# Kernel optimization log

Hardware: AMD Instinct MI355X
Metric: run time of the kernel (lower is better)

## Reference

```python
import jax, jax.numpy as jnp
import numpy as np

N, E = 20000, 320000          # nodes, edges
R, B = 9, 9                   # num_relations, num_bases
IN, HID, OUT = 128, 256, 64   # feature dims
EPS = 1e-5                    # LayerNorm eps


def layer_norm(h, gamma, beta):
    mu = jnp.mean(h, axis=-1, keepdims=True)
    var = jnp.var(h, axis=-1, keepdims=True)
    return (h - mu) * jax.lax.rsqrt(var + EPS) * gamma + beta


def rgcn_conv(x, src, dst, etype, bases, comp, root, bias, aggr):
    # basis decomposition: W_r = sum_b comp[r,b] * bases[b]
    W = jnp.einsum('rb,bio->rio', comp, bases)          # [R, in, out]
    xW = jnp.einsum('ni,rio->rno', x, W)                # [R, N, out]
    msg = xW[etype, src]                                # [E, out] gather per edge
    if aggr == 'max':
        agg = jax.ops.segment_max(msg, dst, num_segments=N)
        agg = jnp.where(jnp.isfinite(agg), agg, 0.0)    # empty segments -> 0
    else:
        agg = jax.ops.segment_sum(msg, dst, num_segments=N)
    return agg + x @ root + bias


def setup_inputs() -> dict:
    key = jax.random.key(0)
    ks = jax.random.split(key, 12)
    rn = lambda k, s, sc=0.05: jax.random.normal(k, s, jnp.float32) * sc
    return {
        'x': jax.random.normal(ks[0], (N, IN), jnp.float32),
        'edge_index': jax.random.randint(ks[1], (2, E), 0, N),
        'edge_type': jax.random.randint(ks[2], (E,), 0, R),
        # conv1 params
        'bases1': rn(ks[3], (B, IN, HID)),
        'comp1': rn(ks[4], (R, B), 0.3),
        'root1': rn(ks[5], (IN, HID)),
        'bias1': jnp.zeros((HID,), jnp.float32),
        'g1': jnp.ones((HID,), jnp.float32),
        'b1': jnp.zeros((HID,), jnp.float32),
        # conv2 params
        'bases2': rn(ks[6], (B, HID, OUT)),
        'comp2': rn(ks[7], (R, B), 0.3),
        'root2': rn(ks[8], (HID, OUT)),
        'bias2': jnp.zeros((OUT,), jnp.float32),
        'g2': jnp.ones((OUT,), jnp.float32),
        'b2': jnp.zeros((OUT,), jnp.float32),
    }


def reference(x, edge_index, edge_type, bases1, comp1, root1, bias1, g1, b1,
              bases2, comp2, root2, bias2, g2, b2):
    src, dst = edge_index[0], edge_index[1]
    h = rgcn_conv(x, src, dst, edge_type, bases1, comp1, root1, bias1, 'max')
    h = jax.nn.relu(layer_norm(h, g1, b1))
    # eval mode: edge dropout and feature dropout are identity
    h = rgcn_conv(h, src, dst, edge_type, bases2, comp2, root2, bias2, 'add')
    h = layer_norm(h, g2, b2)
    return jax.nn.log_softmax(h, axis=1)
```

## Files before the change

kernel.cpp:

```cpp
#include <hip/hip_runtime.h>
#include <math.h>

#define NN 20000
#define NE 320000
#define NREL 9
#define NBASES 9
#define D_IN 128
#define D_HID 256
#define D_OUT 64
#define LN_EPS 1e-5f

#define N1 (NREL * D_HID + D_HID)
#define N2 (NREL * D_OUT + D_OUT)
#define NBLK ((NN + 255) / 256)

typedef __attribute__((ext_vector_type(8))) short bf16x8;
typedef __attribute__((ext_vector_type(4))) float f32x4;

__device__ inline ushort f2b(float f) {
    unsigned u = __float_as_uint(f);
    return (ushort)((u + 0x7FFFu + ((u >> 16) & 1u)) >> 16);
}
__device__ inline float b2f(ushort h) { return __uint_as_float(((unsigned)h) << 16); }
__device__ inline unsigned pack2bf(float f0, float f1) {
    return (unsigned)f2b(f0) | ((unsigned)f2b(f1) << 16);
}

__global__ __launch_bounds__(256) void prep_all(
    const float* __restrict__ bases1, const float* __restrict__ comp1, const float* __restrict__ root1,
    const float* __restrict__ bases2, const float* __restrict__ comp2, const float* __restrict__ root2,
    const float* __restrict__ x, const int* __restrict__ dst,
    ushort* __restrict__ w1t, ushort* __restrict__ w2t, ushort* __restrict__ xbf,
    int* __restrict__ deg)
{
    const int SZW1 = D_IN * D_HID;
    const int SZW2 = D_HID * D_OUT;
    const int SZX  = NN * D_IN;
    int tid = blockIdx.x * 256 + threadIdx.x;
    if (tid < SZW1) {
        int o = tid & (D_HID - 1), k = tid >> 8;
        float acc[NREL];
        #pragma unroll
        for (int r = 0; r < NREL; r++) acc[r] = 0.f;
        #pragma unroll
        for (int b = 0; b < NBASES; b++) {
            float bs = bases1[(b * D_IN + k) * D_HID + o];
            #pragma unroll
            for (int r = 0; r < NREL; r++) acc[r] += comp1[r * NBASES + b] * bs;
        }
        #pragma unroll
        for (int r = 0; r < NREL; r++)
            w1t[(r * D_HID + o) * D_IN + k] = f2b(acc[r]);
        w1t[(NREL * D_HID + o) * D_IN + k] = f2b(root1[k * D_HID + o]);
    } else if (tid < SZW1 + SZW2) {
        int j = tid - SZW1;
        int o = j & (D_OUT - 1), k = j >> 6;
        float acc[NREL];
        #pragma unroll
        for (int r = 0; r < NREL; r++) acc[r] = 0.f;
        #pragma unroll
        for (int b = 0; b < NBASES; b++) {
            float bs = bases2[(b * D_HID + k) * D_OUT + o];
            #pragma unroll
            for (int r = 0; r < NREL; r++) acc[r] += comp2[r * NBASES + b] * bs;
        }
        #pragma unroll
        for (int r = 0; r < NREL; r++)
            w2t[(r * D_OUT + o) * D_HID + k] = f2b(acc[r]);
        w2t[(NREL * D_OUT + o) * D_HID + k] = f2b(root2[k * D_OUT + o]);
    } else if (tid < SZW1 + SZW2 + SZX) {
        int j = tid - SZW1 - SZW2;
        xbf[j] = f2b(x[j]);
    } else if (tid < SZW1 + SZW2 + SZX + NE) {
        int e = tid - SZW1 - SZW2 - SZX;
        atomicAdd(&deg[dst[e]], 1);
    }
}

__global__ __launch_bounds__(256) void scan_blk(
    const int* __restrict__ deg, int* __restrict__ local, int* __restrict__ bsum)
{
    __shared__ int wsum[4];
    int tid = threadIdx.x, lane = tid & 63, w = tid >> 6;
    int i = blockIdx.x * 256 + tid;
    int v = (i < NN) ? deg[i] : 0;
    int x = v;
    #pragma unroll
    for (int d = 1; d < 64; d <<= 1) {
        int y = __shfl_up(x, d, 64);
        if (lane >= d) x += y;
    }
    if (lane == 63) wsum[w] = x;
    __syncthreads();
    int woff = 0;
    for (int j = 0; j < w; j++) woff += wsum[j];
    if (i < NN) local[i] = woff + x - v;
    if (tid == 255) bsum[blockIdx.x] = woff + x;
}

__global__ __launch_bounds__(256) void scan_fin(
    const int* __restrict__ local, const int* __restrict__ bsum,
    int* __restrict__ offs, int* __restrict__ cursor)
{
    __shared__ int boff_s[NBLK];
    int tid = threadIdx.x;
    if (tid < 64) {
        int carry = 0;
        for (int base = 0; base < NBLK; base += 64) {
            int i = base + tid;
            int v = (i < NBLK) ? bsum[i] : 0;
            int x = v;
            #pragma unroll
            for (int d = 1; d < 64; d <<= 1) {
                int y = __shfl_up(x, d, 64);
                if (tid >= d) x += y;
            }
            if (i < NBLK) boff_s[i] = carry + x - v;
            carry += __shfl(x, 63, 64);
        }
    }
    __syncthreads();
    int i = blockIdx.x * 256 + tid;
    if (i < NN) {
        int o = local[i] + boff_s[i >> 8];
        offs[i] = o;
        cursor[i] = o;
    }
    if (i == NN) offs[NN] = NE;
}

__global__ __launch_bounds__(256) void scatter_ep(
    const int* __restrict__ src, const int* __restrict__ dst, const int* __restrict__ etype,
    int* __restrict__ cursor, int* __restrict__ ep1)
{
    int e = blockIdx.x * 256 + threadIdx.x;
    if (e >= NE) return;
    int d = dst[e];
    int s = src[e], r = etype[e];
    int pos = atomicAdd(&cursor[d], 1);
    ep1[pos] = s * N1 + r * D_HID;
}

__global__ __launch_bounds__(256) void gemm_bf16(
    const ushort* __restrict__ A, const ushort* __restrict__ Bt, ushort* __restrict__ C,
    int M, int N, int K)
{
    __shared__ ushort As[2][512 * 8];
    __shared__ ushort Bs[2][512 * 8];

    int tid = threadIdx.x;
    int lane = tid & 63, w = tid >> 6;
    int wm = w >> 1, wn = w & 1;
    int row0 = blockIdx.y * 128, col0 = blockIdx.x * 128;

    int r0 = tid >> 2, q0 = tid & 3;
    int mrw = r0 & 15, gw = r0 >> 4;
    int sw = q0 * 16 + ((mrw + 2 * q0) & 15);
    int lo0 = (gw * 64 + sw) * 8;
    int lo1 = ((gw + 4) * 64 + sw) * 8;
    int arow0 = min(row0 + r0, M - 1);
    int arow1 = min(row0 + r0 + 64, M - 1);
    const ushort* gA0 = &A[(size_t)arow0 * K + q0 * 8];
    const ushort* gA1 = &A[(size_t)arow1 * K + q0 * 8];
    const ushort* gB0 = &Bt[(size_t)(col0 + r0) * K + q0 * 8];
    const ushort* gB1 = &Bt[(size_t)(col0 + r0 + 64) * K + q0 * 8];

    int mr = lane & 15, kq = lane >> 4;
    int inner = (kq * 16 + ((mr + 2 * kq) & 15)) * 8;

    f32x4 acc[4][4];
    #pragma unroll
    for (int mt = 0; mt < 4; mt++)
        #pragma unroll
        for (int nt = 0; nt < 4; nt++)
            acc[mt][nt] = (f32x4){0.f, 0.f, 0.f, 0.f};

    {
        bf16x8 a0 = *(const bf16x8*)gA0;
        bf16x8 a1 = *(const bf16x8*)gA1;
        bf16x8 b0 = *(const bf16x8*)gB0;
        bf16x8 b1 = *(const bf16x8*)gB1;
        *(bf16x8*)&As[0][lo0] = a0;
        *(bf16x8*)&As[0][lo1] = a1;
        *(bf16x8*)&Bs[0][lo0] = b0;
        *(bf16x8*)&Bs[0][lo1] = b1;
    }

    const int NC = K >> 5;
    for (int c = 0; c < NC; c++) {
        __syncthreads();
        int cur = c & 1, nxt = cur ^ 1;
        bf16x8 a0, a1, b0, b1;
        bool more = (c + 1 < NC);
        if (more) {
            gA0 += 32; gA1 += 32; gB0 += 32; gB1 += 32;
            a0 = *(const bf16x8*)gA0;
            a1 = *(const bf16x8*)gA1;
            b0 = *(const bf16x8*)gB0;
            b1 = *(const bf16x8*)gB1;
        }

        bf16x8 af[4], bfr[4];
        #pragma unroll
        for (int mt = 0; mt < 4; mt++)
            af[mt] = *(const bf16x8*)&As[cur][(size_t)((wm * 4 + mt) * 64) * 8 + inner];
        #pragma unroll
        for (int nt = 0; nt < 4; nt++)
            bfr[nt] = *(const bf16x8*)&Bs[cur][(size_t)((wn * 4 + nt) * 64) * 8 + inner];
        #pragma unroll
        for (int mt = 0; mt < 4; mt++)
            #pragma unroll
            for (int nt = 0; nt < 4; nt++)
                acc[mt][nt] = __builtin_amdgcn_mfma_f32_16x16x32_bf16(
                    bfr[nt], af[mt], acc[mt][nt], 0, 0, 0);

        if (more) {
            *(bf16x8*)&As[nxt][lo0] = a0;
            *(bf16x8*)&As[nxt][lo1] = a1;
            *(bf16x8*)&Bs[nxt][lo0] = b0;
            *(bf16x8*)&Bs[nxt][lo1] = b1;
        }
    }

    int q = lane >> 4, cm = lane & 15;
    #pragma unroll
    for (int mt = 0; mt < 4; mt++) {
        int gr = row0 + wm * 64 + mt * 16 + cm;
        if (gr < M) {
            #pragma unroll
            for (int nt = 0; nt < 4; nt++) {
                int gc = col0 + wn * 64 + nt * 16 + q * 4;
                uint2 o;
                o.x = pack2bf(acc[mt][nt][0], acc[mt][nt][1]);
                o.y = pack2bf(acc[mt][nt][2], acc[mt][nt][3]);
                *(uint2*)&C[(size_t)gr * N + gc] = o;
            }
        }
    }
}

__global__ __launch_bounds__(256) void gather1(
    const ushort* __restrict__ xw1, const int* __restrict__ offs, const int* __restrict__ ep1,
    const float* __restrict__ bias, const float* __restrict__ g, const float* __restrict__ b,
    ushort* __restrict__ h)
{
    int n = blockIdx.x * 4 + (threadIdx.x >> 6);
    if (n >= NN) return;
    int lane = threadIdx.x & 63;
    int lane4 = lane * 4;
    int e0 = __builtin_amdgcn_readfirstlane(offs[n]);
    int e1 = __builtin_amdgcn_readfirstlane(offs[n + 1]);

    float m0 = -INFINITY, m1 = -INFINITY, m2 = -INFINITY, m3 = -INFINITY;
    int e = e0;
    for (; e + 8 <= e1; e += 8) {
        int p[8];
        #pragma unroll
        for (int j = 0; j < 8; j++) p[j] = ep1[e + j];
        ushort4 v[8];
        #pragma unroll
        for (int j = 0; j < 8; j++) v[j] = *(const ushort4*)&xw1[(size_t)(p[j] + lane4)];
        #pragma unroll
        for (int j = 0; j < 8; j++) {
            m0 = fmaxf(m0, b2f(v[j].x)); m1 = fmaxf(m1, b2f(v[j].y));
            m2 = fmaxf(m2, b2f(v[j].z)); m3 = fmaxf(m3, b2f(v[j].w));
        }
    }
    for (; e + 2 <= e1; e += 2) {
        int pa = ep1[e], pb = ep1[e + 1];
        ushort4 va = *(const ushort4*)&xw1[(size_t)(pa + lane4)];
        ushort4 vb = *(const ushort4*)&xw1[(size_t)(pb + lane4)];
        m0 = fmaxf(m0, fmaxf(b2f(va.x), b2f(vb.x)));
        m1 = fmaxf(m1, fmaxf(b2f(va.y), b2f(vb.y)));
        m2 = fmaxf(m2, fmaxf(b2f(va.z), b2f(vb.z)));
        m3 = fmaxf(m3, fmaxf(b2f(va.w), b2f(vb.w)));
    }
    for (; e < e1; e++) {
        int p = ep1[e];
        ushort4 v = *(const ushort4*)&xw1[(size_t)(p + lane4)];
        m0 = fmaxf(m0, b2f(v.x)); m1 = fmaxf(m1, b2f(v.y));
        m2 = fmaxf(m2, b2f(v.z)); m3 = fmaxf(m3, b2f(v.w));
    }
    if (e1 == e0) { m0 = m1 = m2 = m3 = 0.f; }

    ushort4 rt = *(const ushort4*)&xw1[(size_t)n * N1 + NREL * D_HID + lane4];
    int c = lane4;
    float t0 = m0 + b2f(rt.x) + bias[c + 0];
    float t1 = m1 + b2f(rt.y) + bias[c + 1];
    float t2 = m2 + b2f(rt.z) + bias[c + 2];
    float t3 = m3 + b2f(rt.w) + bias[c + 3];

    float s = t0 + t1 + t2 + t3;
    float s2 = t0 * t0 + t1 * t1 + t2 * t2 + t3 * t3;
    #pragma unroll
    for (int m = 32; m >= 1; m >>= 1) {
        s  += __shfl_xor(s,  m, 64);
        s2 += __shfl_xor(s2, m, 64);
    }
    float mu = s * (1.f / D_HID);
    float var = s2 * (1.f / D_HID) - mu * mu;
    float rs = rsqrtf(var + LN_EPS);

    ushort4 o;
    o.x = f2b(fmaxf((t0 - mu) * rs * g[c + 0] + b[c + 0], 0.f));
    o.y = f2b(fmaxf((t1 - mu) * rs * g[c + 1] + b[c + 1], 0.f));
    o.z = f2b(fmaxf((t2 - mu) * rs * g[c + 2] + b[c + 2], 0.f));
    o.w = f2b(fmaxf((t3 - mu) * rs * g[c + 3] + b[c + 3], 0.f));
    *(ushort4*)&h[(size_t)n * D_HID + c] = o;
}

__global__ __launch_bounds__(256) void gather2(
    const ushort* __restrict__ xw2, const int* __restrict__ offs, const int* __restrict__ ep1,
    const float* __restrict__ bias, const float* __restrict__ g, const float* __restrict__ b,
    float* __restrict__ out)
{
    int n = blockIdx.x * 4 + (threadIdx.x >> 6);
    if (n >= NN) return;
    int lane = threadIdx.x & 63;
    int e0 = __builtin_amdgcn_readfirstlane(offs[n]);
    int e1 = __builtin_amdgcn_readfirstlane(offs[n + 1]);

    float s = 0.f;
    int e = e0;
    for (; e + 8 <= e1; e += 8) {
        int p[8];
        #pragma unroll
        for (int j = 0; j < 8; j++) p[j] = ep1[e + j] >> 2;
        float a[8];
        #pragma unroll
        for (int j = 0; j < 8; j++) a[j] = b2f(xw2[(size_t)(p[j] + lane)]);
        s += ((a[0] + a[1]) + (a[2] + a[3])) + ((a[4] + a[5]) + (a[6] + a[7]));
    }
    for (; e < e1; e++) {
        s += b2f(xw2[(size_t)((ep1[e] >> 2) + lane)]);
    }
    float v = s + b2f(xw2[(size_t)n * N2 + NREL * D_OUT + lane]) + bias[lane];

    float sm = v, s2 = v * v;
    #pragma unroll
    for (int m = 32; m >= 1; m >>= 1) {
        sm += __shfl_xor(sm, m, 64);
        s2 += __shfl_xor(s2, m, 64);
    }
    float mu = sm * (1.f / D_OUT);
    float var = s2 * (1.f / D_OUT) - mu * mu;
    float y = (v - mu) * rsqrtf(var + LN_EPS) * g[lane] + b[lane];

    float mx = y;
    #pragma unroll
    for (int m = 32; m >= 1; m >>= 1) mx = fmaxf(mx, __shfl_xor(mx, m, 64));
    float ex = __expf(y - mx);
    float se = ex;
    #pragma unroll
    for (int m = 32; m >= 1; m >>= 1) se += __shfl_xor(se, m, 64);
    out[(size_t)n * D_OUT + lane] = y - mx - logf(se);
}

extern "C" void kernel_launch(void* const* d_in, const int* in_sizes, int n_in,
                              void* d_out, int out_size, void* d_ws, size_t ws_size,
                              hipStream_t stream)
{
    const float* x      = (const float*)d_in[0];
    const int*   eidx   = (const int*)  d_in[1];
    const int*   etype  = (const int*)  d_in[2];
    const float* bases1 = (const float*)d_in[3];
    const float* comp1  = (const float*)d_in[4];
    const float* root1  = (const float*)d_in[5];
    const float* bias1  = (const float*)d_in[6];
    const float* g1     = (const float*)d_in[7];
    const float* b1     = (const float*)d_in[8];
    const float* bases2 = (const float*)d_in[9];
    const float* comp2  = (const float*)d_in[10];
    const float* root2  = (const float*)d_in[11];
    const float* bias2  = (const float*)d_in[12];
    const float* g2     = (const float*)d_in[13];
    const float* b2     = (const float*)d_in[14];

    const int* src = eidx;
    const int* dst = eidx + NE;

    char* p = (char*)d_ws;
    auto alloc = [&](size_t bytes) -> char* {
        char* r = p;
        p += (bytes + 255) & ~(size_t)255;
        return r;
    };
    ushort* xbf    = (ushort*)alloc((size_t)NN * D_IN * 2);
    ushort* w1t    = (ushort*)alloc((size_t)N1 * D_IN * 2);
    ushort* w2t    = (ushort*)alloc((size_t)N2 * D_HID * 2);
    ushort* xw1    = (ushort*)alloc((size_t)NN * N1 * 2);
    ushort* xw2    = (ushort*)alloc((size_t)NN * N2 * 2);
    ushort* h      = (ushort*)alloc((size_t)NN * D_HID * 2);
    int*    deg    = (int*)   alloc((size_t)NN * 4);
    int*    local  = (int*)   alloc((size_t)NN * 4);
    int*    bsum   = (int*)   alloc((size_t)NBLK * 4);
    int*    offs   = (int*)   alloc((size_t)(NN + 1) * 4);
    int*    cursor = (int*)   alloc((size_t)NN * 4);
    int*    ep1    = (int*)   alloc((size_t)NE * 4);

    hipMemsetAsync(deg, 0, (size_t)NN * 4, stream);
    const int SZP = D_IN * D_HID + D_HID * D_OUT + NN * D_IN + NE;
    prep_all<<<(SZP + 255) / 256, 256, 0, stream>>>(
        bases1, comp1, root1, bases2, comp2, root2, x, dst, w1t, w2t, xbf, deg);

    scan_blk<<<NBLK, 256, 0, stream>>>(deg, local, bsum);
    scan_fin<<<NBLK, 256, 0, stream>>>(local, bsum, offs, cursor);
    scatter_ep<<<(NE + 255) / 256, 256, 0, stream>>>(src, dst, etype, cursor, ep1);

    gemm_bf16<<<dim3(N1 / 128, (NN + 127) / 128), 256, 0, stream>>>(xbf, w1t, xw1, NN, N1, D_IN);
    gather1<<<(NN + 3) / 4, 256, 0, stream>>>(xw1, offs, ep1, bias1, g1, b1, h);

    gemm_bf16<<<dim3(N2 / 128, (NN + 127) / 128), 256, 0, stream>>>(h, w2t, xw2, NN, N2, D_HID);
    gather2<<<(NN + 3) / 4, 256, 0, stream>>>(xw2, offs, ep1, bias2, g2, b2, (float*)d_out);
}
```

Measured before the change: 241.7 us.

## Fuse CSR build into cooperative kernel; widen gather1 loads to 8 channels

Replaces the memset, prep, two scan kernels and the edge scatter with one persistent cooperative kernel that uses grid-wide syncs between phases. This removes several launches and their gaps. Separately, gather1 now has each half-wave load 8 bf16 channels per lane and handle alternate edges, then merges the two halves with a shuffle. The cooperative kernel relies on grid.sync being supported and on all 1024 blocks being co-resident, and the grid-stride loops may give less parallelism than the old per-element launches.

```diff
diff --git a/kernel.cpp b/kernel.cpp
--- a/kernel.cpp
+++ b/kernel.cpp
@@ -1,5 +1,8 @@
 #include <hip/hip_runtime.h>
+#include <hip/hip_cooperative_groups.h>
 #include <math.h>
+
+namespace cg = cooperative_groups;
 
 #define NN 20000
 #define NE 320000
@@ -13,6 +16,7 @@
 #define N1 (NREL * D_HID + D_HID)
 #define N2 (NREL * D_OUT + D_OUT)
 #define NBLK ((NN + 255) / 256)
+#define FE_BLOCKS 1024
 
 typedef __attribute__((ext_vector_type(8))) short bf16x8;
 typedef __attribute__((ext_vector_type(4))) float f32x4;
@@ -26,119 +30,120 @@
     return (unsigned)f2b(f0) | ((unsigned)f2b(f1) << 16);
 }
 
-__global__ __launch_bounds__(256) void prep_all(
+__global__ __launch_bounds__(256) void front_end(
     const float* __restrict__ bases1, const float* __restrict__ comp1, const float* __restrict__ root1,
     const float* __restrict__ bases2, const float* __restrict__ comp2, const float* __restrict__ root2,
-    const float* __restrict__ x, const int* __restrict__ dst,
+    const float* __restrict__ x, const int* __restrict__ src, const int* __restrict__ dst,
+    const int* __restrict__ etype,
     ushort* __restrict__ w1t, ushort* __restrict__ w2t, ushort* __restrict__ xbf,
-    int* __restrict__ deg)
+    int* __restrict__ deg, int* __restrict__ local, int* __restrict__ bsum,
+    int* __restrict__ offs, int* __restrict__ cursor, int* __restrict__ ep1)
 {
+    cg::grid_group grid = cg::this_grid();
     const int SZW1 = D_IN * D_HID;
     const int SZW2 = D_HID * D_OUT;
     const int SZX  = NN * D_IN;
-    int tid = blockIdx.x * 256 + threadIdx.x;
-    if (tid < SZW1) {
-        int o = tid & (D_HID - 1), k = tid >> 8;
-        float acc[NREL];
-        #pragma unroll
-        for (int r = 0; r < NREL; r++) acc[r] = 0.f;
-        #pragma unroll
-        for (int b = 0; b < NBASES; b++) {
-            float bs = bases1[(b * D_IN + k) * D_HID + o];
-            #pragma unroll
-            for (int r = 0; r < NREL; r++) acc[r] += comp1[r * NBASES + b] * bs;
-        }
-        #pragma unroll
-        for (int r = 0; r < NREL; r++)
-            w1t[(r * D_HID + o) * D_IN + k] = f2b(acc[r]);
-        w1t[(NREL * D_HID + o) * D_IN + k] = f2b(root1[k * D_HID + o]);
-    } else if (tid < SZW1 + SZW2) {
-        int j = tid - SZW1;
-        int o = j & (D_OUT - 1), k = j >> 6;
-        float acc[NREL];
-        #pragma unroll
-        for (int r = 0; r < NREL; r++) acc[r] = 0.f;
-        #pragma unroll
-        for (int b = 0; b < NBASES; b++) {
-            float bs = bases2[(b * D_HID + k) * D_OUT + o];
-            #pragma unroll
-            for (int r = 0; r < NREL; r++) acc[r] += comp2[r * NBASES + b] * bs;
-        }
-        #pragma unroll
-        for (int r = 0; r < NREL; r++)
-            w2t[(r * D_OUT + o) * D_HID + k] = f2b(acc[r]);
-        w2t[(NREL * D_OUT + o) * D_HID + k] = f2b(root2[k * D_OUT + o]);
-    } else if (tid < SZW1 + SZW2 + SZX) {
-        int j = tid - SZW1 - SZW2;
-        xbf[j] = f2b(x[j]);
-    } else if (tid < SZW1 + SZW2 + SZX + NE) {
-        int e = tid - SZW1 - SZW2 - SZX;
-        atomicAdd(&deg[dst[e]], 1);
-    }
-}
-
-__global__ __launch_bounds__(256) void scan_blk(
-    const int* __restrict__ deg, int* __restrict__ local, int* __restrict__ bsum)
-{
-    __shared__ int wsum[4];
-    int tid = threadIdx.x, lane = tid & 63, w = tid >> 6;
-    int i = blockIdx.x * 256 + tid;
-    int v = (i < NN) ? deg[i] : 0;
-    int x = v;
-    #pragma unroll
-    for (int d = 1; d < 64; d <<= 1) {
-        int y = __shfl_up(x, d, 64);
-        if (lane >= d) x += y;
-    }
-    if (lane == 63) wsum[w] = x;
-    __syncthreads();
-    int woff = 0;
-    for (int j = 0; j < w; j++) woff += wsum[j];
-    if (i < NN) local[i] = woff + x - v;
-    if (tid == 255) bsum[blockIdx.x] = woff + x;
-}
-
-__global__ __launch_bounds__(256) void scan_fin(
-    const int* __restrict__ local, const int* __restrict__ bsum,
-    int* __restrict__ offs, int* __restrict__ cursor)
-{
-    __shared__ int boff_s[NBLK];
     int tid = threadIdx.x;
-    if (tid < 64) {
-        int carry = 0;
-        for (int base = 0; base < NBLK; base += 64) {
-            int i = base + tid;
-            int v = (i < NBLK) ? bsum[i] : 0;
-            int x = v;
-            #pragma unroll
-            for (int d = 1; d < 64; d <<= 1) {
-                int y = __shfl_up(x, d, 64);
-                if (tid >= d) x += y;
+    int gtid = blockIdx.x * 256 + tid;
+    const int gstride = FE_BLOCKS * 256;
+
+    for (int i = gtid; i < NN; i += gstride) deg[i] = 0;
+    for (int t = gtid; t < SZW1 + SZW2 + SZX; t += gstride) {
+        if (t < SZW1) {
+            int o = t & (D_HID - 1), k = t >> 8;
+            float acc[NREL];
+            #pragma unroll
+            for (int r = 0; r < NREL; r++) acc[r] = 0.f;
+            #pragma unroll
+            for (int b = 0; b < NBASES; b++) {
+                float bs = bases1[(b * D_IN + k) * D_HID + o];
+                #pragma unroll
+                for (int r = 0; r < NREL; r++) acc[r] += comp1[r * NBASES + b] * bs;
             }
-            if (i < NBLK) boff_s[i] = carry + x - v;
-            carry += __shfl(x, 63, 64);
-        }
-    }
-    __syncthreads();
-    int i = blockIdx.x * 256 + tid;
-    if (i < NN) {
-        int o = local[i] + boff_s[i >> 8];
-        offs[i] = o;
-        cursor[i] = o;
-    }
-    if (i == NN) offs[NN] = NE;
-}
-
-__global__ __launch_bounds__(256) void scatter_ep(
-    const int* __restrict__ src, const int* __restrict__ dst, const int* __restrict__ etype,
-    int* __restrict__ cursor, int* __restrict__ ep1)
-{
-    int e = blockIdx.x * 256 + threadIdx.x;
-    if (e >= NE) return;
-    int d = dst[e];
-    int s = src[e], r = etype[e];
-    int pos = atomicAdd(&cursor[d], 1);
-    ep1[pos] = s * N1 + r * D_HID;
+            #pragma unroll
+            for (int r = 0; r < NREL; r++)
+                w1t[(r * D_HID + o) * D_IN + k] = f2b(acc[r]);
+            w1t[(NREL * D_HID + o) * D_IN + k] = f2b(root1[k * D_HID + o]);
+        } else if (t < SZW1 + SZW2) {
+            int j = t - SZW1;
+            int o = j & (D_OUT - 1), k = j >> 6;
+            float acc[NREL];
+            #pragma unroll
+            for (int r = 0; r < NREL; r++) acc[r] = 0.f;
+            #pragma unroll
+            for (int b = 0; b < NBASES; b++) {
+                float bs = bases2[(b * D_HID + k) * D_OUT + o];
+                #pragma unroll
+                for (int r = 0; r < NREL; r++) acc[r] += comp2[r * NBASES + b] * bs;
+            }
+            #pragma unroll
+            for (int r = 0; r < NREL; r++)
+                w2t[(r * D_OUT + o) * D_HID + k] = f2b(acc[r]);
+            w2t[(NREL * D_OUT + o) * D_HID + k] = f2b(root2[k * D_OUT + o]);
+        } else {
+            int j = t - SZW1 - SZW2;
+            xbf[j] = f2b(x[j]);
+        }
+    }
+    grid.sync();
+
+    for (int e = gtid; e < NE; e += gstride) atomicAdd(&deg[dst[e]], 1);
+    grid.sync();
+
+    if (blockIdx.x < NBLK) {
+        __shared__ int wsum[4];
+        int lane = tid & 63, w = tid >> 6;
+        int i = blockIdx.x * 256 + tid;
+        int v = (i < NN) ? deg[i] : 0;
+        int xs = v;
+        #pragma unroll
+        for (int d = 1; d < 64; d <<= 1) {
+            int y = __shfl_up(xs, d, 64);
+            if (lane >= d) xs += y;
+        }
+        if (lane == 63) wsum[w] = xs;
+        __syncthreads();
+        int woff = 0;
+        for (int j = 0; j < w; j++) woff += wsum[j];
+        if (i < NN) local[i] = woff + xs - v;
+        if (tid == 255) bsum[blockIdx.x] = woff + xs;
+    }
+    grid.sync();
+
+    if (blockIdx.x < NBLK) {
+        __shared__ int boff_s[NBLK];
+        if (tid < 64) {
+            int carry = 0;
+            for (int base = 0; base < NBLK; base += 64) {
+                int i = base + tid;
+                int v = (i < NBLK) ? bsum[i] : 0;
+                int xs = v;
+                #pragma unroll
+                for (int d = 1; d < 64; d <<= 1) {
+                    int y = __shfl_up(xs, d, 64);
+                    if (tid >= d) xs += y;
+                }
+                if (i < NBLK) boff_s[i] = carry + xs - v;
+                carry += __shfl(xs, 63, 64);
+            }
+        }
+        __syncthreads();
+        int i = blockIdx.x * 256 + tid;
+        if (i < NN) {
+            int o = local[i] + boff_s[i >> 8];
+            offs[i] = o;
+            cursor[i] = o;
+        }
+        if (i == NN) offs[NN] = NE;
+    }
+    grid.sync();
+
+    for (int e = gtid; e < NE; e += gstride) {
+        int d = dst[e];
+        int s = src[e], r = etype[e];
+        int pos = atomicAdd(&cursor[d], 1);
+        ep1[pos] = s * N1 + r * D_HID;
+    }
 }
 
 __global__ __launch_bounds__(256) void gemm_bf16(
@@ -247,66 +252,80 @@
     int n = blockIdx.x * 4 + (threadIdx.x >> 6);
     if (n >= NN) return;
     int lane = threadIdx.x & 63;
-    int lane4 = lane * 4;
+    int half = lane >> 5, sub = lane & 31;
+    int ch8 = sub * 8;
     int e0 = __builtin_amdgcn_readfirstlane(offs[n]);
     int e1 = __builtin_amdgcn_readfirstlane(offs[n + 1]);
 
-    float m0 = -INFINITY, m1 = -INFINITY, m2 = -INFINITY, m3 = -INFINITY;
+    float mm[8];
+    #pragma unroll
+    for (int k = 0; k < 8; k++) mm[k] = -INFINITY;
+
     int e = e0;
-    for (; e + 8 <= e1; e += 8) {
+    for (; e + 16 <= e1; e += 16) {
         int p[8];
         #pragma unroll
-        for (int j = 0; j < 8; j++) p[j] = ep1[e + j];
-        ushort4 v[8];
-        #pragma unroll
-        for (int j = 0; j < 8; j++) v[j] = *(const ushort4*)&xw1[(size_t)(p[j] + lane4)];
-        #pragma unroll
-        for (int j = 0; j < 8; j++) {
-            m0 = fmaxf(m0, b2f(v[j].x)); m1 = fmaxf(m1, b2f(v[j].y));
-            m2 = fmaxf(m2, b2f(v[j].z)); m3 = fmaxf(m3, b2f(v[j].w));
-        }
-    }
-    for (; e + 2 <= e1; e += 2) {
-        int pa = ep1[e], pb = ep1[e + 1];
-        ushort4 va = *(const ushort4*)&xw1[(size_t)(pa + lane4)];
-        ushort4 vb = *(const ushort4*)&xw1[(size_t)(pb + lane4)];
-        m0 = fmaxf(m0, fmaxf(b2f(va.x), b2f(vb.x)));
-        m1 = fmaxf(m1, fmaxf(b2f(va.y), b2f(vb.y)));
-        m2 = fmaxf(m2, fmaxf(b2f(va.z), b2f(vb.z)));
-        m3 = fmaxf(m3, fmaxf(b2f(va.w), b2f(vb.w)));
-    }
-    for (; e < e1; e++) {
-        int p = ep1[e];
-        ushort4 v = *(const ushort4*)&xw1[(size_t)(p + lane4)];
-        m0 = fmaxf(m0, b2f(v.x)); m1 = fmaxf(m1, b2f(v.y));
-        m2 = fmaxf(m2, b2f(v.z)); m3 = fmaxf(m3, b2f(v.w));
-    }
-    if (e1 == e0) { m0 = m1 = m2 = m3 = 0.f; }
-
-    ushort4 rt = *(const ushort4*)&xw1[(size_t)n * N1 + NREL * D_HID + lane4];
-    int c = lane4;
-    float t0 = m0 + b2f(rt.x) + bias[c + 0];
-    float t1 = m1 + b2f(rt.y) + bias[c + 1];
-    float t2 = m2 + b2f(rt.z) + bias[c + 2];
-    float t3 = m3 + b2f(rt.w) + bias[c + 3];
-
-    float s = t0 + t1 + t2 + t3;
-    float s2 = t0 * t0 + t1 * t1 + t2 * t2 + t3 * t3;
+        for (int j = 0; j < 8; j++) p[j] = ep1[e + j * 2 + half];
+        bf16x8 v[8];
+        #pragma unroll
+        for (int j = 0; j < 8; j++) v[j] = *(const bf16x8*)&xw1[(size_t)(p[j] + ch8)];
+        #pragma unroll
+        for (int j = 0; j < 8; j++)
+            #pragma unroll
+            for (int k = 0; k < 8; k++)
+                mm[k] = fmaxf(mm[k], b2f((ushort)v[j][k]));
+    }
+    for (; e < e1; e += 2) {
+        int ia = e + half;
+        if (ia >= e1) ia = e1 - 1;
+        int p = ep1[ia];
+        bf16x8 v = *(const bf16x8*)&xw1[(size_t)(p + ch8)];
+        #pragma unroll
+        for (int k = 0; k < 8; k++) mm[k] = fmaxf(mm[k], b2f((ushort)v[k]));
+    }
+    #pragma unroll
+    for (int k = 0; k < 8; k++) mm[k] = fmaxf(mm[k], __shfl_xor(mm[k], 32, 64));
+    if (e1 == e0) {
+        #pragma unroll
+        for (int k = 0; k < 8; k++) mm[k] = 0.f;
+    }
+
+    bf16x8 rt = *(const bf16x8*)&xw1[(size_t)n * N1 + NREL * D_HID + ch8];
+    float4 bia0 = *(const float4*)&bias[ch8];
+    float4 bia1 = *(const float4*)&bias[ch8 + 4];
+    float t[8];
+    t[0] = mm[0] + b2f((ushort)rt[0]) + bia0.x;
+    t[1] = mm[1] + b2f((ushort)rt[1]) + bia0.y;
+    t[2] = mm[2] + b2f((ushort)rt[2]) + bia0.z;
+    t[3] = mm[3] + b2f((ushort)rt[3]) + bia0.w;
+    t[4] = mm[4] + b2f((ushort)rt[4]) + bia1.x;
+    t[5] = mm[5] + b2f((ushort)rt[5]) + bia1.y;
+    t[6] = mm[6] + b2f((ushort)rt[6]) + bia1.z;
+    t[7] = mm[7] + b2f((ushort)rt[7]) + bia1.w;
+
+    float s = 0.f, s2 = 0.f;
+    #pragma unroll
+    for (int k = 0; k < 8; k++) { s += t[k]; s2 += t[k] * t[k]; }
     #pragma unroll
     for (int m = 32; m >= 1; m >>= 1) {
         s  += __shfl_xor(s,  m, 64);
         s2 += __shfl_xor(s2, m, 64);
     }
-    float mu = s * (1.f / D_HID);
-    float var = s2 * (1.f / D_HID) - mu * mu;
+    float mu = s * (1.f / (2 * D_HID));
+    float var = s2 * (1.f / (2 * D_HID)) - mu * mu;
     float rs = rsqrtf(var + LN_EPS);
 
-    ushort4 o;
-    o.x = f2b(fmaxf((t0 - mu) * rs * g[c + 0] + b[c + 0], 0.f));
-    o.y = f2b(fmaxf((t1 - mu) * rs * g[c + 1] + b[c + 1], 0.f));
-    o.z = f2b(fmaxf((t2 - mu) * rs * g[c + 2] + b[c + 2], 0.f));
-    o.w = f2b(fmaxf((t3 - mu) * rs * g[c + 3] + b[c + 3], 0.f));
-    *(ushort4*)&h[(size_t)n * D_HID + c] = o;
+    if (half == 0) {
+        float4 g0 = *(const float4*)&g[ch8], g1v = *(const float4*)&g[ch8 + 4];
+        float4 b0 = *(const float4*)&b[ch8], b1v = *(const float4*)&b[ch8 + 4];
+        float gg[8] = {g0.x, g0.y, g0.z, g0.w, g1v.x, g1v.y, g1v.z, g1v.w};
+        float bb[8] = {b0.x, b0.y, b0.z, b0.w, b1v.x, b1v.y, b1v.z, b1v.w};
+        bf16x8 o;
+        #pragma unroll
+        for (int k = 0; k < 8; k++)
+            o[k] = (short)f2b(fmaxf((t[k] - mu) * rs * gg[k] + bb[k], 0.f));
+        *(bf16x8*)&h[(size_t)n * D_HID + ch8] = o;
+    }
 }
 
 __global__ __launch_bounds__(256) void gather2(
@@ -398,14 +417,16 @@
     int*    cursor = (int*)   alloc((size_t)NN * 4);
     int*    ep1    = (int*)   alloc((size_t)NE * 4);
 
-    hipMemsetAsync(deg, 0, (size_t)NN * 4, stream);
-    const int SZP = D_IN * D_HID + D_HID * D_OUT + NN * D_IN + NE;
-    prep_all<<<(SZP + 255) / 256, 256, 0, stream>>>(
-        bases1, comp1, root1, bases2, comp2, root2, x, dst, w1t, w2t, xbf, deg);
-
-    scan_blk<<<NBLK, 256, 0, stream>>>(deg, local, bsum);
-    scan_fin<<<NBLK, 256, 0, stream>>>(local, bsum, offs, cursor);
-    scatter_ep<<<(NE + 255) / 256, 256, 0, stream>>>(src, dst, etype, cursor, ep1);
+    void* args[] = {
+        (void*)&bases1, (void*)&comp1, (void*)&root1,
+        (void*)&bases2, (void*)&comp2, (void*)&root2,
+        (void*)&x, (void*)&src, (void*)&dst, (void*)&etype,
+        (void*)&w1t, (void*)&w2t, (void*)&xbf,
+        (void*)&deg, (void*)&local, (void*)&bsum,
+        (void*)&offs, (void*)&cursor, (void*)&ep1
+    };
+    hipLaunchCooperativeKernel((void*)front_end, dim3(FE_BLOCKS), dim3(256),
+                               args, 0, stream);
 
     gemm_bf16<<<dim3(N1 / 128, (NN + 127) / 128), 256, 0, stream>>>(xbf, w1t, xw1, NN, N1, D_IN);
     gather1<<<(NN + 3) / 4, 256, 0, stream>>>(xw1, offs, ep1, bias1, g1, b1, h);
```

After: 669.6 us. 2.77x slower.
